# Performance work log

Hardware: AMD Instinct MI355X
Metric: run time of the kernel (lower is better)

## Reference

```python
import jax, jax.numpy as jnp
import numpy as np

N = 10000        # num nodes
E = 640000       # num edges
FIN = 128        # input feature dim
NH = 8           # num heads
FOUT = 16        # out features per head (NH*FOUT == FIN)
NEG_SLOPE = 0.2
EPS = 1e-16


def setup_inputs() -> dict:
    key = jax.random.key(0)
    ks = jax.random.split(key, 7)
    x = jax.random.normal(ks[0], (N, FIN), dtype=jnp.float32)
    edges = jax.random.randint(ks[1], (2, E), 0, N, dtype=jnp.int64)
    # kaiming-uniform-ish init scale
    s = float(np.sqrt(6.0 / FIN))
    W_proj = jax.random.uniform(ks[2], (NH * FOUT, FIN), minval=-s, maxval=s, dtype=jnp.float32)
    W_skip = jax.random.uniform(ks[3], (NH * FOUT, FIN), minval=-s, maxval=s, dtype=jnp.float32)
    sf = float(np.sqrt(6.0 / FOUT))
    score_src = jax.random.uniform(ks[4], (1, NH, FOUT), minval=-sf, maxval=sf, dtype=jnp.float32)
    score_tgt = jax.random.uniform(ks[5], (1, NH, FOUT), minval=-sf, maxval=sf, dtype=jnp.float32)
    bias = jnp.zeros((NH * FOUT,), dtype=jnp.float32)
    return {"x": x, "edges": edges, "W_proj": W_proj, "W_skip": W_skip,
            "score_src": score_src, "score_tgt": score_tgt, "bias": bias}


def reference(x, edges, W_proj, W_skip, score_src, score_tgt, bias):
    src, tgt = edges[0], edges[1]
    # project: [N, NH, FOUT]
    proj = (x @ W_proj.T).reshape(N, NH, FOUT)
    # per-node scores: [N, NH]
    s_src = (proj * score_src).sum(-1)
    s_tgt = (proj * score_tgt).sum(-1)
    # lift to edges and score: [E, NH]
    scores = jax.nn.leaky_relu(s_src[src] + s_tgt[tgt], negative_slope=NEG_SLOPE)
    # neighborhood-aware softmax (global max subtraction, as in original)
    exp_scores = jnp.exp(scores - jnp.max(scores))
    denom = jax.ops.segment_sum(exp_scores, tgt, num_segments=N)  # [N, NH]
    att = exp_scores / (denom[tgt] + EPS)                          # [E, NH]
    # weighted aggregation: [N, NH, FOUT]
    weighted = proj[src] * att[:, :, None]
    out = jax.ops.segment_sum(weighted, tgt, num_segments=N)
    # skip connection (dims differ per-head, so skip_proj is used), concat, bias
    out = out + (x @ W_skip.T).reshape(N, NH, FOUT)
    out = out.reshape(N, NH * FOUT) + bias
    return out
```

## Files before the change

kernel.cpp:

```cpp
#include <hip/hip_runtime.h>
#include <hip/hip_bf16.h>

#define FIN   128
#define NH    8
#define NEG   0.2f
#define HB    64
#define NMAX  10240

typedef __attribute__((ext_vector_type(8))) short short8;
typedef __attribute__((ext_vector_type(4))) float f32x4;

__device__ __forceinline__ short f2bf(float f) {
    unsigned u = __float_as_uint(f);
    return (short)((u + 0x7FFFu + ((u >> 16) & 1u)) >> 16);
}
__device__ __forceinline__ float bflo(unsigned p) { return __uint_as_float(p << 16); }
__device__ __forceinline__ float bfhi(unsigned p) { return __uint_as_float(p & 0xFFFF0000u); }
__device__ __forceinline__ float ld_f(const void* p, int i, bool bf16) {
    if (bf16) {
        unsigned h = ((const unsigned short*)p)[i];
        return __uint_as_float(h << 16);
    }
    return ((const float*)p)[i];
}
__device__ __forceinline__ short8 ld_frag(const void* p, size_t off, bool bf16) {
    if (bf16) return *(const short8*)((const short*)p + off);
    const float* f = (const float*)p + off;
    f32x4 f0 = *(const f32x4*)f;
    f32x4 f1 = *(const f32x4*)(f + 4);
    short8 r;
    r[0] = f2bf(f0[0]); r[1] = f2bf(f0[1]); r[2] = f2bf(f0[2]); r[3] = f2bf(f0[3]);
    r[4] = f2bf(f1[0]); r[5] = f2bf(f1[1]); r[6] = f2bf(f1[2]); r[7] = f2bf(f1[3]);
    return r;
}
__device__ __forceinline__ float escore(float ss, float st) {
    float v = ss + st;
    v = v > 0.f ? v : NEG * v;
    return __expf(fminf(v, 60.f));
}
__device__ __forceinline__ bool wave_bf16(const unsigned* x32) {
    unsigned w  = x32[threadIdx.x & 63];
    unsigned ex = (w >> 7) & 0xFFu;
    return __popcll(__ballot(ex >= 118u && ex <= 130u)) >= 48;
}
__device__ __forceinline__ bool wave_e64(const int* e32) {
    return __popcll(__ballot(e32[2 * (threadIdx.x & 63) + 1] == 0)) == 64;
}

__global__ __launch_bounds__(256) void k_projhist(
    const void* __restrict__ x, const void* __restrict__ Wp,
    const void* __restrict__ Ws,
    const void* __restrict__ ssrcw, const void* __restrict__ stgtw,
    unsigned short* __restrict__ projb, float* __restrict__ skip,
    float* __restrict__ s_src, float* __restrict__ s_tgt,
    const int* __restrict__ e32, int* __restrict__ hist2d,
    int N, int E, int tiles, int halfTiles, int projBlocks, int perB)
{
    __shared__ int lhist[NMAX];
    if ((int)blockIdx.x >= projBlocks) {
        const bool e64 = wave_e64(e32);
        const int hb = (int)blockIdx.x - projBlocks;
        const int t = threadIdx.x;
        for (int j = t; j < N; j += 256) lhist[j] = 0;
        __syncthreads();
        const int lo = hb * perB;
        const int hi = min(lo + perB, E);
        for (int i = lo + t; i < hi; i += 256) {
            int tg = e64 ? e32[2 * ((size_t)E + i)] : e32[(size_t)E + i];
            atomicAdd(&lhist[tg], 1);
        }
        __syncthreads();
        for (int j = t; j < N; j += 256) hist2d[(size_t)hb * N + j] = lhist[j];
        return;
    }
    const bool bf16 = wave_bf16((const unsigned*)x);
    const int lane = threadIdx.x & 63;
    const int wt = blockIdx.x * 4 + (threadIdx.x >> 6);
    if (wt >= tiles) return;
    const int mat = (wt >= halfTiles) ? 1 : 0;
    const int m0 = (mat ? wt - halfTiles : wt) * 16;
    const int mr = lane & 15;
    const int kb = lane >> 4;

    short8 a[4];
    const size_t xoff = (size_t)(m0 + mr) * FIN + kb * 8;
#pragma unroll
    for (int s = 0; s < 4; ++s) a[s] = ld_frag(x, xoff + s * 32, bf16);

    const void* W = mat ? Ws : Wp;
    f32x4 acc[8];
#pragma unroll
    for (int c = 0; c < 8; ++c) {
        acc[c] = (f32x4){0.f, 0.f, 0.f, 0.f};
        const size_t woff = (size_t)(c * 16 + mr) * FIN + kb * 8;
#pragma unroll
        for (int s = 0; s < 4; ++s) {
            short8 b = ld_frag(W, woff + s * 32, bf16);
            acc[c] = __builtin_amdgcn_mfma_f32_16x16x32_bf16(a[s], b, acc[c], 0, 0, 0);
        }
    }
    if (mat == 0) {
#pragma unroll
        for (int c = 0; c < 8; ++c) {
            float sw = ld_f(ssrcw, c * 16 + mr, bf16);
            float tw = ld_f(stgtw, c * 16 + mr, bf16);
#pragma unroll
            for (int r = 0; r < 4; ++r) {
                int row = m0 + kb * 4 + r;
                float v = acc[c][r];
                projb[(size_t)row * FIN + c * 16 + mr] = (unsigned short)f2bf(v);
                float vs = v * sw, vt = v * tw;
#pragma unroll
                for (int o = 8; o >= 1; o >>= 1) {
                    vs += __shfl_xor(vs, o);
                    vt += __shfl_xor(vt, o);
                }
                if (mr == 0) {
                    s_src[row * NH + c] = vs;
                    s_tgt[row * NH + c] = vt;
                }
            }
        }
    } else {
#pragma unroll
        for (int c = 0; c < 8; ++c)
#pragma unroll
            for (int r = 0; r < 4; ++r)
                skip[(size_t)(m0 + kb * 4 + r) * FIN + c * 16 + mr] = acc[c][r];
    }
}

__global__ __launch_bounds__(256) void k_colscan(
    const int* __restrict__ hist2d, int* __restrict__ pbase,
    int* __restrict__ cnt, int N)
{
    int j = blockIdx.x * 256 + threadIdx.x;
    if (j >= N) return;
    int s = 0;
#pragma unroll 4
    for (int b = 0; b < HB; ++b) {
        int v = hist2d[(size_t)b * N + j];
        pbase[(size_t)b * N + j] = s;
        s += v;
    }
    cnt[j] = s;
}

__global__ __launch_bounds__(256) void k_offscan(const int* __restrict__ cnt,
                                                 int* __restrict__ offs, int N)
{
    const int t = threadIdx.x;
    const int PER = (N + 255) / 256;
    const int base = t * PER;
    int local[40];
    int sum = 0;
    for (int i = 0; i < PER && i < 40; ++i) {
        int idx = base + i;
        int v = (idx < N) ? cnt[idx] : 0;
        local[i] = sum;
        sum += v;
    }
    __shared__ int sd[256];
    sd[t] = sum;
    __syncthreads();
#pragma unroll
    for (int off = 1; off < 256; off <<= 1) {
        int add = (t >= off) ? sd[t - off] : 0;
        __syncthreads();
        sd[t] += add;
        __syncthreads();
    }
    int excl = sd[t] - sum;
    for (int i = 0; i < PER && i < 40; ++i) {
        int idx = base + i;
        if (idx < N) offs[idx] = excl + local[i];
    }
    if (t == 255) offs[N] = sd[255];
}

__global__ __launch_bounds__(256) void k_place(
    const int* __restrict__ e32, const int* __restrict__ offs,
    const int* __restrict__ pbase, int* __restrict__ sorted_src,
    int N, int E, int perB)
{
    __shared__ int cur[NMAX];
    const bool e64 = wave_e64(e32);
    const int b = blockIdx.x, t = threadIdx.x;
    for (int j = t; j < N; j += 256)
        cur[j] = offs[j] + pbase[(size_t)b * N + j];
    __syncthreads();
    const int lo = b * perB;
    const int hi = min(lo + perB, E);
    for (int i = lo + t; i < hi; i += 256) {
        int s, tg;
        if (e64) { s = e32[2 * (size_t)i]; tg = e32[2 * ((size_t)E + i)]; }
        else     { s = e32[i];             tg = e32[(size_t)E + i]; }
        int pos = atomicAdd(&cur[tg], 1);
        sorted_src[pos] = s;
    }
}

__global__ __launch_bounds__(64) void k_aggregate(
    const int* __restrict__ offs, const int* __restrict__ sorted_src,
    const float* __restrict__ s_src, const float* __restrict__ s_tgt,
    const unsigned short* __restrict__ projb, const float* __restrict__ skip,
    const void* __restrict__ bias, void* __restrict__ out,
    const unsigned* __restrict__ x32)
{
    const bool bf16 = wave_bf16(x32);
    const int n = blockIdx.x, l = threadIdx.x;
    const int start = offs[n], end = offs[n + 1];
    const int h = l >> 3;
    const int c2 = l * 2;
    const float st = s_tgt[(size_t)n * NH + h];

    float ae0 = 0.f, ao0 = 0.f, ae1 = 0.f, ao1 = 0.f;
    float ae2 = 0.f, ao2 = 0.f, ae3 = 0.f, ao3 = 0.f;
    float d0 = 0.f, d1 = 0.f, d2 = 0.f, d3 = 0.f;
    int e = start;
    for (; e + 4 <= end; e += 4) {
        int s0 = sorted_src[e],     s1 = sorted_src[e + 1];
        int s2 = sorted_src[e + 2], s3 = sorted_src[e + 3];
        float w0 = escore(s_src[(size_t)s0 * NH + h], st);
        float w1 = escore(s_src[(size_t)s1 * NH + h], st);
        float w2 = escore(s_src[(size_t)s2 * NH + h], st);
        float w3 = escore(s_src[(size_t)s3 * NH + h], st);
        unsigned p0 = *(const unsigned*)(projb + (size_t)s0 * FIN + c2);
        unsigned p1 = *(const unsigned*)(projb + (size_t)s1 * FIN + c2);
        unsigned p2 = *(const unsigned*)(projb + (size_t)s2 * FIN + c2);
        unsigned p3 = *(const unsigned*)(projb + (size_t)s3 * FIN + c2);
        ae0 += w0 * bflo(p0); ao0 += w0 * bfhi(p0); d0 += w0;
        ae1 += w1 * bflo(p1); ao1 += w1 * bfhi(p1); d1 += w1;
        ae2 += w2 * bflo(p2); ao2 += w2 * bfhi(p2); d2 += w2;
        ae3 += w3 * bflo(p3); ao3 += w3 * bfhi(p3); d3 += w3;
    }
    for (; e < end; ++e) {
        int s = sorted_src[e];
        float w = escore(s_src[(size_t)s * NH + h], st);
        unsigned p = *(const unsigned*)(projb + (size_t)s * FIN + c2);
        ae0 += w * bflo(p); ao0 += w * bfhi(p); d0 += w;
    }

    float inv = 1.f / (((d0 + d1) + (d2 + d3)) + 1e-16f);
    float2 sk = *(const float2*)(skip + (size_t)n * FIN + c2);
    float be, bo;
    if (bf16) {
        unsigned bb = *(const unsigned*)((const unsigned short*)bias + c2);
        be = bflo(bb); bo = bfhi(bb);
    } else {
        float2 b2 = *(const float2*)((const float*)bias + c2);
        be = b2.x; bo = b2.y;
    }
    float oe = ((ae0 + ae1) + (ae2 + ae3)) * inv + sk.x + be;
    float oo = ((ao0 + ao1) + (ao2 + ao3)) * inv + sk.y + bo;
    if (bf16) {
        unsigned pr = ((unsigned)(unsigned short)f2bf(oo) << 16)
                    | (unsigned)(unsigned short)f2bf(oe);
        ((unsigned*)out)[((size_t)n * FIN + c2) >> 1] = pr;
    } else {
        float2 o2; o2.x = oe; o2.y = oo;
        *(float2*)((float*)out + (size_t)n * FIN + c2) = o2;
    }
}

extern "C" void kernel_launch(void* const* d_in, const int* in_sizes, int n_in,
                              void* d_out, int out_size, void* d_ws, size_t ws_size,
                              hipStream_t stream)
{
    const void* x    = d_in[0];
    const int* edges = (const int*)d_in[1];
    const void* Wp   = d_in[2];
    const void* Ws   = d_in[3];
    const void* ssw  = d_in[4];
    const void* stw  = d_in[5];
    const void* bias = d_in[6];

    const int N = in_sizes[0] / FIN;
    const int E = in_sizes[1] / 2;

    unsigned short* projb = (unsigned short*)d_ws;
    float* skip     = (float*)(projb + (size_t)N * FIN);
    float* s_src    = skip + (size_t)N * FIN;
    float* s_tgt    = s_src + (size_t)N * NH;
    int* sorted_src = (int*)(s_tgt + (size_t)N * NH);
    int* offs       = sorted_src + E;
    int* cnt        = offs + (N + 1);
    int* hist2d     = cnt + N;
    int* pbase      = hist2d + (size_t)HB * N;

    const int halfTiles  = (N + 15) / 16;
    const int tiles      = 2 * halfTiles;
    const int projBlocks = (tiles + 3) / 4;
    const int perB       = (E + HB - 1) / HB;

    k_projhist<<<projBlocks + HB, 256, 0, stream>>>(
        x, Wp, Ws, ssw, stw, projb, skip, s_src, s_tgt,
        edges, hist2d, N, E, tiles, halfTiles, projBlocks, perB);
    k_colscan<<<(N + 255) / 256, 256, 0, stream>>>(hist2d, pbase, cnt, N);
    k_offscan<<<1, 256, 0, stream>>>(cnt, offs, N);
    k_place<<<HB, 256, 0, stream>>>(edges, offs, pbase, sorted_src, N, E, perB);
    k_aggregate<<<N, 64, 0, stream>>>(offs, sorted_src, s_src, s_tgt, projb,
                                      skip, bias, d_out, (const unsigned*)x);
}
```

Before: 166.9 us.

## Store skip projection in bf16, pack histogram counters, double histogram blocks

The skip projection is now stored as bf16 rather than fp32, which halves its write in the projection kernel and its read in the aggregate kernel. The per-block histogram packs two 16-bit counters per 32-bit LDS word, halving LDS use. The number of histogram/placement blocks doubles to 128, giving more parallelism in the histogram and place kernels but making the column scan longer. The trade-offs are bf16 rounding error in the skip term, and 16-bit counters that could overflow if one target ever received more than 65535 edges within a single block.

```diff
diff --git a/kernel.cpp b/kernel.cpp
--- a/kernel.cpp
+++ b/kernel.cpp
@@ -4,7 +4,7 @@
 #define FIN   128
 #define NH    8
 #define NEG   0.2f
-#define HB    64
+#define HB    128
 #define NMAX  10240
 
 typedef __attribute__((ext_vector_type(8))) short short8;
@@ -51,26 +51,28 @@
     const void* __restrict__ x, const void* __restrict__ Wp,
     const void* __restrict__ Ws,
     const void* __restrict__ ssrcw, const void* __restrict__ stgtw,
-    unsigned short* __restrict__ projb, float* __restrict__ skip,
+    unsigned short* __restrict__ projb, unsigned short* __restrict__ skipb,
     float* __restrict__ s_src, float* __restrict__ s_tgt,
     const int* __restrict__ e32, int* __restrict__ hist2d,
     int N, int E, int tiles, int halfTiles, int projBlocks, int perB)
 {
-    __shared__ int lhist[NMAX];
+    __shared__ unsigned l32[NMAX / 2];
     if ((int)blockIdx.x >= projBlocks) {
         const bool e64 = wave_e64(e32);
         const int hb = (int)blockIdx.x - projBlocks;
         const int t = threadIdx.x;
-        for (int j = t; j < N; j += 256) lhist[j] = 0;
+        const int nw = (N + 1) >> 1;
+        for (int j = t; j < nw; j += 256) l32[j] = 0;
         __syncthreads();
         const int lo = hb * perB;
         const int hi = min(lo + perB, E);
         for (int i = lo + t; i < hi; i += 256) {
             int tg = e64 ? e32[2 * ((size_t)E + i)] : e32[(size_t)E + i];
-            atomicAdd(&lhist[tg], 1);
+            atomicAdd(&l32[tg >> 1], 1u << ((tg & 1) << 4));
         }
         __syncthreads();
-        for (int j = t; j < N; j += 256) hist2d[(size_t)hb * N + j] = lhist[j];
+        for (int j = t; j < N; j += 256)
+            hist2d[(size_t)hb * N + j] = (l32[j >> 1] >> ((j & 1) << 4)) & 0xFFFFu;
         return;
     }
     const bool bf16 = wave_bf16((const unsigned*)x);
@@ -126,7 +128,8 @@
         for (int c = 0; c < 8; ++c)
 #pragma unroll
             for (int r = 0; r < 4; ++r)
-                skip[(size_t)(m0 + kb * 4 + r) * FIN + c * 16 + mr] = acc[c][r];
+                skipb[(size_t)(m0 + kb * 4 + r) * FIN + c * 16 + mr] =
+                    (unsigned short)f2bf(acc[c][r]);
     }
 }
 
@@ -203,7 +206,7 @@
 __global__ __launch_bounds__(64) void k_aggregate(
     const int* __restrict__ offs, const int* __restrict__ sorted_src,
     const float* __restrict__ s_src, const float* __restrict__ s_tgt,
-    const unsigned short* __restrict__ projb, const float* __restrict__ skip,
+    const unsigned short* __restrict__ projb, const unsigned short* __restrict__ skipb,
     const void* __restrict__ bias, void* __restrict__ out,
     const unsigned* __restrict__ x32)
 {
@@ -242,7 +245,7 @@
     }
 
     float inv = 1.f / (((d0 + d1) + (d2 + d3)) + 1e-16f);
-    float2 sk = *(const float2*)(skip + (size_t)n * FIN + c2);
+    unsigned skp = *(const unsigned*)(skipb + (size_t)n * FIN + c2);
     float be, bo;
     if (bf16) {
         unsigned bb = *(const unsigned*)((const unsigned short*)bias + c2);
@@ -251,8 +254,8 @@
         float2 b2 = *(const float2*)((const float*)bias + c2);
         be = b2.x; bo = b2.y;
     }
-    float oe = ((ae0 + ae1) + (ae2 + ae3)) * inv + sk.x + be;
-    float oo = ((ao0 + ao1) + (ao2 + ao3)) * inv + sk.y + bo;
+    float oe = ((ae0 + ae1) + (ae2 + ae3)) * inv + bflo(skp) + be;
+    float oo = ((ao0 + ao1) + (ao2 + ao3)) * inv + bfhi(skp) + bo;
     if (bf16) {
         unsigned pr = ((unsigned)(unsigned short)f2bf(oo) << 16)
                     | (unsigned)(unsigned short)f2bf(oe);
@@ -279,8 +282,8 @@
     const int E = in_sizes[1] / 2;
 
     unsigned short* projb = (unsigned short*)d_ws;
-    float* skip     = (float*)(projb + (size_t)N * FIN);
-    float* s_src    = skip + (size_t)N * FIN;
+    unsigned short* skipb = projb + (size_t)N * FIN;
+    float* s_src    = (float*)(skipb + (size_t)N * FIN);
     float* s_tgt    = s_src + (size_t)N * NH;
     int* sorted_src = (int*)(s_tgt + (size_t)N * NH);
     int* offs       = sorted_src + E;
@@ -294,11 +297,11 @@
     const int perB       = (E + HB - 1) / HB;
 
     k_projhist<<<projBlocks + HB, 256, 0, stream>>>(
-        x, Wp, Ws, ssw, stw, projb, skip, s_src, s_tgt,
+        x, Wp, Ws, ssw, stw, projb, skipb, s_src, s_tgt,
         edges, hist2d, N, E, tiles, halfTiles, projBlocks, perB);
     k_colscan<<<(N + 255) / 256, 256, 0, stream>>>(hist2d, pbase, cnt, N);
     k_offscan<<<1, 256, 0, stream>>>(cnt, offs, N);
     k_place<<<HB, 256, 0, stream>>>(edges, offs, pbase, sorted_src, N, E, perB);
     k_aggregate<<<N, 64, 0, stream>>>(offs, sorted_src, s_src, s_tgt, projb,
-                                      skip, bias, d_out, (const unsigned*)x);
-}
+                                      skipb, bias, d_out, (const unsigned*)x);
+}
```

Result: no change. 165.9 us (-0.6%).
